# Kernel tuning notes

Hardware: AMD Instinct MI355X
Metric: run time of the kernel (lower is better)

The kernel has to match this reference:

```python
import jax, jax.numpy as jnp
import numpy as np

HEADS = 16
DIM_HEAD = 64


def setup_inputs() -> dict:
    key = jax.random.key(0)
    k1, k2, k3 = jax.random.split(key, 3)
    b, n, dim = 2, 2048, 1024
    x = jax.random.normal(k1, (b, n, dim), dtype=jnp.float32)
    W_qkv = jax.random.normal(k2, (dim, 6 * HEADS * DIM_HEAD), dtype=jnp.float32) * 0.02
    W_out = jax.random.normal(k3, (HEADS * DIM_HEAD, dim), dtype=jnp.float32) * 0.02
    return {"x": x, "W_qkv": W_qkv, "W_out": W_out}


def reference(x, W_qkv, W_out):
    b, n, _ = x.shape
    h, d = HEADS, DIM_HEAD
    scale = d ** -0.5

    # project and split into 6 head-wise tensors: (qkv h d) grouping order
    qkv = (x @ W_qkv).reshape(b, n, 6, h, d).transpose(2, 0, 3, 1, 4)  # [6,b,h,n,d]
    qu, ku, vu, qc, kc, vc = qkv
    qu_s = qu * scale
    qc_s = qc * scale

    idx = jnp.arange(n)
    future = idx[None, :] > idx[:, None]  # torch triu(1): True strictly above diag

    # term1: qc . vu, zeroed on future positions
    term1 = jnp.einsum('bhid,bhjd->bhij', qc_s, vu)
    term1 = jnp.where(future, 0.0, term1)

    # sigmoid lookahead attention, kept ONLY on strictly-future positions
    lookahead = jax.nn.sigmoid(jnp.einsum('bhid,bhjd->bhij', qu_s, ku))
    lookahead = jnp.where(future, lookahead, 0.0)

    # Su[i,k] = sum_j term1[i,j] * lookahead[k,j]
    Su = jnp.einsum('bhij,bhkj->bhik', term1, lookahead)
    Sc = jnp.einsum('bhid,bhjd->bhij', qc_s, kc)

    scores = Sc - jax.nn.silu(Su)
    neg = -jnp.finfo(scores.dtype).max
    scores = jnp.where(future, neg, scores)

    attn = jax.nn.softmax(scores, axis=-1)
    out = jnp.einsum('bhij,bhjd->bhid', attn, vc)  # [b,h,n,d]

    out = out.transpose(0, 2, 1, 3).reshape(b, n, h * d)
    return out @ W_out
```

## Files before the change

### kernel.cpp

```cpp
#include <hip/hip_runtime.h>
#include <hip/hip_bf16.h>
#include <stdint.h>


typedef unsigned short u16;
typedef __attribute__((ext_vector_type(8))) short s8v;
typedef __attribute__((ext_vector_type(4))) float f4v;

__device__ __forceinline__ u16 f2bf(float f) {
  union { float f; unsigned u; } v; v.f = f;
  unsigned r = v.u + 0x7FFFu + ((v.u >> 16) & 1u);
  return (u16)(r >> 16);
}
__device__ __forceinline__ float bf2f(u16 u) {
  union { unsigned u; float f; } v; v.u = ((unsigned)u) << 16; return v.f;
}

typedef __attribute__((address_space(1))) const void* gas_t;
typedef __attribute__((address_space(3))) void* las_t;
__device__ __forceinline__ void gld16(const void* g, void* l) {
  __builtin_amdgcn_global_load_lds((gas_t)g, (las_t)l, 16, 0, 0);
}

__device__ __forceinline__ void zero_acc(f4v acc[4][4]) {
  f4v z = {0.f, 0.f, 0.f, 0.f};
#pragma unroll
  for (int m = 0; m < 4; ++m)
#pragma unroll
    for (int n = 0; n < 4; ++n) acc[m][n] = z;
}


__global__ void convert_x_kernel(const float* __restrict__ in, u16* __restrict__ out) {
  int i = (blockIdx.x * 256 + threadIdx.x) * 4;
  float4 v = *(const float4*)(&in[i]);
  out[i + 0] = f2bf(v.x);
  out[i + 1] = f2bf(v.y);
  out[i + 2] = f2bf(v.z);
  out[i + 3] = f2bf(v.w);
}

__global__ void transpose_convert_kernel(const float* __restrict__ in, u16* __restrict__ out,
                                         int R, int C) {
  __shared__ float tile[32][33];
  int c0 = blockIdx.x * 32, r0 = blockIdx.y * 32;
  for (int rr = threadIdx.y; rr < 32; rr += 8)
    tile[rr][threadIdx.x] = in[(size_t)(r0 + rr) * C + (c0 + threadIdx.x)];
  __syncthreads();
  for (int cc = threadIdx.y; cc < 32; cc += 8)
    out[(size_t)(c0 + cc) * R + (r0 + threadIdx.x)] = f2bf(tile[threadIdx.x][cc]);
}


__global__ __launch_bounds__(256, 2) void gemm_qkv_kernel(
    const u16* __restrict__ xb, const u16* __restrict__ wqkvT,
    u16* __restrict__ quS, u16* __restrict__ ku, u16* __restrict__ vu,
    u16* __restrict__ qcS, u16* __restrict__ kc, u16* __restrict__ vcN) {
  __shared__ u16 sA[2][8192];
  __shared__ u16 sB[2][8192];
  int bm = blockIdx.x, bn = blockIdx.y;
  int tid = threadIdx.x, lane = tid & 63, w = tid >> 6, wm = w >> 1, wn = w & 1;
  int g = lane >> 4, l15 = lane & 15;
  const int sz = (l15 & 7) << 3;
  const int bo = tid * 16;

  const u16* Ab = xb + (size_t)(bm * 128) * 1024;
  const u16* Bb = wqkvT + (size_t)(bn * 128) * 1024;

  auto stg = [&](const u16* base, int ks, u16* dst) {
#pragma unroll
    for (int it = 0; it < 4; ++it) {
      int o = bo + it * 4096;
      int row = o >> 7, lo = o & 127;
      gld16(base + (size_t)row * 1024 + ks * 64 + ((lo ^ ((row & 7) << 4)) >> 1),
            (char*)dst + o);
    }
  };

  f4v acc[4][4];
  zero_acc(acc);
  stg(Ab, 0, sA[0]);
  stg(Bb, 0, sB[0]);
  stg(Ab, 1, sA[1]);
  stg(Bb, 1, sB[1]);

  for (int ks = 0; ks < 16; ++ks) {
    int buf = ks & 1;
    if (ks < 15)
      asm volatile("s_waitcnt vmcnt(8)" ::: "memory");
    else
      asm volatile("s_waitcnt vmcnt(0)" ::: "memory");
    __builtin_amdgcn_sched_barrier(0);
    __builtin_amdgcn_s_barrier();
    __builtin_amdgcn_sched_barrier(0);
#pragma unroll
    for (int kk = 0; kk < 2; ++kk) {
      int c2 = kk * 32 + g * 8;
      s8v a[4], b[4];
#pragma unroll
      for (int m = 0; m < 4; ++m)
        a[m] = *(const s8v*)(&sA[buf][(wm * 64 + m * 16 + l15) * 64 + (c2 ^ sz)]);
#pragma unroll
      for (int n = 0; n < 4; ++n)
        b[n] = *(const s8v*)(&sB[buf][(wn * 64 + n * 16 + l15) * 64 + (c2 ^ sz)]);
#pragma unroll
      for (int m = 0; m < 4; ++m)
#pragma unroll
        for (int n = 0; n < 4; ++n)
          acc[m][n] = __builtin_amdgcn_mfma_f32_16x16x32_bf16(a[m], b[n], acc[m][n], 0, 0, 0);
    }
    __builtin_amdgcn_s_barrier();
    if (ks + 2 < 16) {
      stg(Ab, ks + 2, sA[buf]);
      stg(Bb, ks + 2, sB[buf]);
    }
  }

  int s = bn >> 3;
  int b = bm >> 4;
  int nn0 = (bm & 15) * 128;
  int hh0 = (bn & 7) * 2;
  float scale = (s == 0 || s == 3) ? 0.125f : 1.f;
  u16* obase;
  switch (s) {
    case 0: obase = quS; break;
    case 1: obase = ku; break;
    case 2: obase = vu; break;
    case 3: obase = qcS; break;
    case 4: obase = kc; break;
    default: obase = vcN; break;
  }
  u16* sE = (u16*)sA;
#pragma unroll
  for (int pass = 0; pass < 2; ++pass) {
    __syncthreads();
    if (wn == pass) {
#pragma unroll
      for (int m = 0; m < 4; ++m)
#pragma unroll
        for (int n = 0; n < 4; ++n)
#pragma unroll
          for (int j = 0; j < 4; ++j) {
            int lrow = wm * 64 + m * 16 + g * 4 + j;
            int d = n * 16 + l15;
            sE[lrow * 64 + d] = f2bf(acc[m][n][j] * scale);
          }
    }
    __syncthreads();
    int bh = (b << 4) + hh0 + pass;
    u16* dst = obase + ((size_t)bh * 2048 + nn0) * 64;
    for (int it = 0; it < 4; ++it) {
      int e = (tid + it * 256) * 8;
      *(uint4*)(dst + e) = *(const uint4*)(&sE[e]);
    }
  }
}


__global__ __launch_bounds__(256) void transpose_v_kernel(const u16* __restrict__ vcN,
                                                          u16* __restrict__ vcT) {
  __shared__ u16 t[64][72];
  int nt = blockIdx.x, bh = blockIdx.y;
  const u16* src = vcN + ((size_t)bh * 2048 + nt * 64) * 64;
  int tid = threadIdx.x;
  for (int i = tid; i < 512; i += 256) {
    int r = i >> 3, cseg = i & 7;
    *(uint4*)(&t[r][cseg * 8]) = *(const uint4*)(src + r * 64 + cseg * 8);
  }
  __syncthreads();
  u16* dst = vcT + (size_t)bh * 64 * 2048 + nt * 64;
  for (int i = tid; i < 512; i += 256) {
    int d = i >> 3, nseg = i & 7;
    u16 tmp[8];
#pragma unroll
    for (int e = 0; e < 8; ++e) tmp[e] = t[nseg * 8 + e][d];
    *(uint4*)(dst + (size_t)d * 2048 + nseg * 8) = *(uint4*)tmp;
  }
}


__global__ __launch_bounds__(256, 2) void tl_kernel(
    const u16* __restrict__ qcS, const u16* __restrict__ vu,
    const u16* __restrict__ quS, const u16* __restrict__ ku,
    u16* __restrict__ term1p, u16* __restrict__ lookp, int c0) {
  __shared__ u16 S[32768];
  int t = blockIdx.x, lb = blockIdx.y, bh = c0 + lb;
  int I = 0;
  while ((I + 1) * (I + 2) / 2 <= t) ++I;
  int K = t - I * (I + 1) / 2;
  int tid = threadIdx.x, lane = tid & 63, w = tid >> 6, wm = w >> 1, wn = w & 1;
  int g = lane >> 4, l15 = lane & 15;
  const int sz = (l15 & 7) << 3;
  const int bo = tid * 16;

  auto stg = [&](const u16* base, int rt, u16* dst) {
#pragma unroll
    for (int it = 0; it < 4; ++it) {
      int o = bo + it * 4096;
      int row = o >> 7, lo = o & 127;
      gld16(base + ((size_t)bh * 2048 + rt * 128 + row) * 64 + ((lo ^ ((row & 7) << 4)) >> 1),
            (char*)dst + o);
    }
  };
  stg(qcS, I, S);
  stg(vu, K, S + 8192);
  stg(quS, K, S + 16384);
  stg(ku, I, S + 24576);

  asm volatile("s_waitcnt vmcnt(0)" ::: "memory");
  __builtin_amdgcn_sched_barrier(0);
  __syncthreads();

  f4v acc1[4][4], acc2[4][4];
  zero_acc(acc1);
  zero_acc(acc2);
#pragma unroll
  for (int kk = 0; kk < 2; ++kk) {
    int c2 = kk * 32 + g * 8;
    s8v a1[4], b1[4], a2[4], b2[4];
#pragma unroll
    for (int m = 0; m < 4; ++m) {
      a1[m] = *(const s8v*)(&S[(wm * 64 + m * 16 + l15) * 64 + (c2 ^ sz)]);
      a2[m] = *(const s8v*)(&S[16384 + (wm * 64 + m * 16 + l15) * 64 + (c2 ^ sz)]);
    }
#pragma unroll
    for (int n = 0; n < 4; ++n) {
      b1[n] = *(const s8v*)(&S[8192 + (wn * 64 + n * 16 + l15) * 64 + (c2 ^ sz)]);
      b2[n] = *(const s8v*)(&S[24576 + (wn * 64 + n * 16 + l15) * 64 + (c2 ^ sz)]);
    }
#pragma unroll
    for (int m = 0; m < 4; ++m)
#pragma unroll
      for (int n = 0; n < 4; ++n) {
        acc1[m][n] = __builtin_amdgcn_mfma_f32_16x16x32_bf16(a1[m], b1[n], acc1[m][n], 0, 0, 0);
        acc2[m][n] = __builtin_amdgcn_mfma_f32_16x16x32_bf16(a2[m], b2[n], acc2[m][n], 0, 0, 0);
      }
  }
  __syncthreads();

#pragma unroll
  for (int m = 0; m < 4; ++m)
#pragma unroll
    for (int n = 0; n < 4; ++n)
#pragma unroll
      for (int j4 = 0; j4 < 4; ++j4) {
        int lr = wm * 64 + m * 16 + g * 4 + j4;
        int lc = wn * 64 + n * 16 + l15;
        int idx = wn * 8192 + lr * 64 + ((lc & 63) ^ ((lr & 7) << 3));
        float v1 = acc1[m][n][j4];
        v1 = ((K * 128 + lc) > (I * 128 + lr)) ? 0.f : v1;
        S[idx] = f2bf(v1);
        float v2 = acc2[m][n][j4];
        v2 = ((I * 128 + lc) > (K * 128 + lr)) ? (1.f / (1.f + __expf(-v2))) : 0.f;
        S[16384 + idx] = f2bf(v2);
      }
  __syncthreads();

  u16* o1 = term1p + ((size_t)lb * 136 + t) * 16384;
  u16* o2 = lookp + ((size_t)lb * 136 + t) * 16384;
#pragma unroll
  for (int it = 0; it < 8; ++it) {
    int e = (tid + it * 256) * 8;
    *(uint4*)(o1 + e) = *(const uint4*)(&S[e]);
    *(uint4*)(o2 + e) = *(const uint4*)(&S[16384 + e]);
  }
}


__global__ __launch_bounds__(256, 2) void castle_kernel(
    const u16* __restrict__ term1p, const u16* __restrict__ lookp,
    const u16* __restrict__ qcS, const u16* __restrict__ kc,
    const u16* __restrict__ vcT,
    u16* __restrict__ opart, float* __restrict__ ml, int c0) {
  __shared__ u16 sA[16384];
  __shared__ u16 sB[16384];
  int bid = blockIdx.x;
  int lb = bid / 136, sid = bid % 136;
  int bh = c0 + lb;
  int I = 15, rem = sid;
  while (rem > I) { rem -= I + 1; --I; }
  int K = rem;
  int t = I * (I + 1) / 2 + K;

  int tid = threadIdx.x, lane = tid & 63, w = tid >> 6;
  int g = lane >> 4, l15 = lane & 15;
  const int sz = (l15 & 7) << 3;

  const char* t1b = (const char*)(term1p + (size_t)lb * 136 * 16384);
  const char* lkb = (const char*)(lookp + (size_t)lb * 136 * 16384);
  const int IT = I * (I + 1) / 2;
  const int bo = tid * 16;

  s8v qa[2][2];
#pragma unroll
  for (int mg = 0; mg < 2; ++mg)
#pragma unroll
    for (int kk = 0; kk < 2; ++kk)
      qa[mg][kk] = *(const s8v*)(&qcS[((size_t)bh * 2048 + I * 128 + w * 32 + mg * 16 + l15) * 64 +
                                      kk * 32 + g * 8]);

  f4v su[2][8];
  {
    f4v z = {0.f, 0.f, 0.f, 0.f};
#pragma unroll
    for (int mg = 0; mg < 2; ++mg)
#pragma unroll
      for (int n = 0; n < 8; ++n) su[mg][n] = z;
  }

  auto stage = [&](int h, int buf) {
    int j = h >> 1, hf = h & 1;
    const char* srcA = t1b + (size_t)(IT + j) * 32768 + hf * 16384;
    const char* srcB = lkb + (size_t)(j * (j + 1) / 2 + K) * 32768 + hf * 16384;
    char* dA = (char*)sA + buf * 16384;
    char* dB = (char*)sB + buf * 16384;
#pragma unroll
    for (int it = 0; it < 4; ++it) {
      gld16(srcA + bo + it * 4096, dA + bo + it * 4096);
      gld16(srcB + bo + it * 4096, dB + bo + it * 4096);
    }
  };

  const int h0 = 2 * K, h1 = 2 * I + 1;
  stage(h0, 0);
  for (int h = h0; h <= h1; ++h) {
    int cur = (h - h0) & 1;
    if (h < h1) {
      stage(h + 1, cur ^ 1);
      asm volatile("s_waitcnt vmcnt(8)" ::: "memory");
    } else {
      asm volatile("s_waitcnt vmcnt(0)" ::: "memory");
    }
    __builtin_amdgcn_sched_barrier(0);
    __builtin_amdgcn_s_barrier();
    __builtin_amdgcn_sched_barrier(0);
    const u16* bA = sA + cur * 8192;
    const u16* bB = sB + cur * 8192;
    __builtin_amdgcn_s_setprio(1);
#pragma unroll
    for (int kk = 0; kk < 2; ++kk) {
      int c2 = kk * 32 + g * 8;
      s8v a[2], b[8];
      a[0] = *(const s8v*)(&bA[(w * 32 + l15) * 64 + (c2 ^ sz)]);
      a[1] = *(const s8v*)(&bA[(w * 32 + 16 + l15) * 64 + (c2 ^ sz)]);
#pragma unroll
      for (int n = 0; n < 8; ++n)
        b[n] = *(const s8v*)(&bB[(n * 16 + l15) * 64 + (c2 ^ sz)]);
#pragma unroll
      for (int mg = 0; mg < 2; ++mg)
#pragma unroll
        for (int n = 0; n < 8; ++n)
          su[mg][n] = __builtin_amdgcn_mfma_f32_16x16x32_bf16(a[mg], b[n], su[mg][n], 0, 0, 0);
    }
    __builtin_amdgcn_s_setprio(0);
    __builtin_amdgcn_s_barrier();
  }

  {
#pragma unroll
    for (int it = 0; it < 4; ++it) {
      int o = bo + it * 4096;
      int kh = o >> 13, oc = o & 8191;
      int dr = oc >> 7, lo = oc & 127;
      const u16* src = vcT + ((size_t)bh * 64 + dr) * 2048 + K * 128 + kh * 64 +
                       ((lo ^ ((dr & 7) << 4)) >> 1);
      gld16(src, (char*)sB + o);
    }
#pragma unroll
    for (int it = 0; it < 4; ++it) {
      int o = bo + it * 4096;
      int row = o >> 7, lo = o & 127;
      const u16* src = kc + ((size_t)bh * 2048 + K * 128 + row) * 64 +
                       ((lo ^ ((row & 7) << 4)) >> 1);
      gld16(src, (char*)sB + 16384 + o);
    }
  }
#pragma unroll
  for (int mg = 0; mg < 2; ++mg)
#pragma unroll
    for (int n = 0; n < 8; ++n)
#pragma unroll
      for (int j4 = 0; j4 < 4; ++j4) {
        float xv = su[mg][n][j4];
        su[mg][n][j4] = -(xv / (1.f + __expf(-xv)));
      }
  __syncthreads();

#pragma unroll
  for (int kk = 0; kk < 2; ++kk) {
    int c = kk * 32 + g * 8;
    s8v b[8];
#pragma unroll
    for (int n = 0; n < 8; ++n)
      b[n] = *(const s8v*)(&sB[8192 + (n * 16 + l15) * 64 + (c ^ sz)]);
#pragma unroll
    for (int mg = 0; mg < 2; ++mg)
#pragma unroll
      for (int n = 0; n < 8; ++n)
        su[mg][n] = __builtin_amdgcn_mfma_f32_16x16x32_bf16(qa[mg][kk], b[n], su[mg][n], 0, 0, 0);
  }

  if (K == I) {
#pragma unroll
    for (int mg = 0; mg < 2; ++mg)
#pragma unroll
      for (int n = 0; n < 8; ++n)
#pragma unroll
        for (int j4 = 0; j4 < 4; ++j4) {
          int lr = w * 32 + mg * 16 + g * 4 + j4;
          int lc = n * 16 + l15;
          if (lc > lr) su[mg][n][j4] = -3.0e38f;
        }
  }

  float mrow[2][4], lrow[2][4];
#pragma unroll
  for (int mg = 0; mg < 2; ++mg)
#pragma unroll
    for (int j4 = 0; j4 < 4; ++j4) {
      float v = -3.0e38f;
#pragma unroll
      for (int n = 0; n < 8; ++n) v = fmaxf(v, su[mg][n][j4]);
      v = fmaxf(v, __shfl_xor(v, 1));
      v = fmaxf(v, __shfl_xor(v, 2));
      v = fmaxf(v, __shfl_xor(v, 4));
      v = fmaxf(v, __shfl_xor(v, 8));
      mrow[mg][j4] = v;
    }
#pragma unroll
  for (int mg = 0; mg < 2; ++mg)
#pragma unroll
    for (int j4 = 0; j4 < 4; ++j4) {
      float sum = 0.f;
      int prow = w * 32 + mg * 16 + g * 4 + j4;
      int psz = ((g * 4 + j4) & 7) << 3;
#pragma unroll
      for (int n = 0; n < 8; ++n) {
        float e = __expf(su[mg][n][j4] - mrow[mg][j4]);
        sum += e;
        int pc = n * 16 + l15;
        sA[(n >> 2) * 8192 + prow * 64 + ((pc & 63) ^ psz)] = f2bf(e);
      }
      sum += __shfl_xor(sum, 1);
      sum += __shfl_xor(sum, 2);
      sum += __shfl_xor(sum, 4);
      sum += __shfl_xor(sum, 8);
      lrow[mg][j4] = sum;
    }
  __syncthreads();

  f4v o[2][4];
  {
    f4v z = {0.f, 0.f, 0.f, 0.f};
#pragma unroll
    for (int mg = 0; mg < 2; ++mg)
#pragma unroll
      for (int nd = 0; nd < 4; ++nd) o[mg][nd] = z;
  }
#pragma unroll
  for (int kk = 0; kk < 4; ++kk) {
    int kh = kk >> 1;
    int cc = (kk & 1) * 32 + g * 8;
    s8v pa[2], vb[4];
#pragma unroll
    for (int mg = 0; mg < 2; ++mg)
      pa[mg] = *(const s8v*)(&sA[kh * 8192 + (w * 32 + mg * 16 + l15) * 64 + (cc ^ sz)]);
#pragma unroll
    for (int nd = 0; nd < 4; ++nd)
      vb[nd] = *(const s8v*)(&sB[kh * 4096 + (nd * 16 + l15) * 64 + (cc ^ sz)]);
#pragma unroll
    for (int mg = 0; mg < 2; ++mg)
#pragma unroll
      for (int nd = 0; nd < 4; ++nd)
        o[mg][nd] = __builtin_amdgcn_mfma_f32_16x16x32_bf16(pa[mg], vb[nd], o[mg][nd], 0, 0, 0);
  }

  size_t tb = (size_t)lb * 136 + t;
#pragma unroll
  for (int mg = 0; mg < 2; ++mg)
#pragma unroll
    for (int nd = 0; nd < 4; ++nd)
#pragma unroll
      for (int j4 = 0; j4 < 4; ++j4) {
        int prow = w * 32 + mg * 16 + g * 4 + j4;
        int dcol = nd * 16 + l15;
        opart[(tb * 128 + prow) * 64 + dcol] = f2bf(o[mg][nd][j4]);
      }
  if (l15 == 0) {
#pragma unroll
    for (int mg = 0; mg < 2; ++mg)
#pragma unroll
      for (int j4 = 0; j4 < 4; ++j4) {
        int prow = w * 32 + mg * 16 + g * 4 + j4;
        ml[tb * 256 + prow] = mrow[mg][j4];
        ml[tb * 256 + 128 + prow] = lrow[mg][j4];
      }
  }
}


__global__ __launch_bounds__(256) void combine_kernel(const u16* __restrict__ opart,
                                                      const float* __restrict__ ml,
                                                      u16* __restrict__ attn, int c0) {
  int lb = blockIdx.x, I = blockIdx.y, bh = c0 + lb;
  int tid = threadIdx.x;
  int row = tid >> 1, dh = (tid & 1) << 5;
  float M = -3.0e38f, L = 0.f;
  float O[32];
#pragma unroll
  for (int i = 0; i < 32; ++i) O[i] = 0.f;
  for (int K = 0; K <= I; ++K) {
    size_t tb = (size_t)lb * 136 + I * (I + 1) / 2 + K;
    float m = ml[tb * 256 + row];
    float l = ml[tb * 256 + 128 + row];
    float newM = fmaxf(M, m);
    float so = __expf(M - newM), sn = __expf(m - newM);
    L = L * so + l * sn;
    const u16* op = opart + (tb * 128 + row) * 64 + dh;
#pragma unroll
    for (int q = 0; q < 4; ++q) {
      s8v ov = *(const s8v*)(op + q * 8);
#pragma unroll
      for (int e = 0; e < 8; ++e)
        O[q * 8 + e] = O[q * 8 + e] * so + bf2f((u16)ov[e]) * sn;
    }
    M = newM;
  }
  float inv = 1.f / L;
  int b = bh >> 4, hh = bh & 15;
  u16* dst = attn + ((size_t)b * 2048 + I * 128 + row) * 1024 + hh * 64 + dh;
#pragma unroll
  for (int i = 0; i < 32; ++i) dst[i] = f2bf(O[i] * inv);
}


__global__ __launch_bounds__(256, 2) void gemm_out_kernel(const u16* __restrict__ attn,
                                                          const u16* __restrict__ woutT,
                                                          float* __restrict__ out) {
  __shared__ u16 sA[2][8192];
  __shared__ u16 sB[2][8192];
  int bm = blockIdx.x, bn = blockIdx.y;
  int tid = threadIdx.x, lane = tid & 63, w = tid >> 6, wm = w >> 1, wn = w & 1;
  int g = lane >> 4, l15 = lane & 15;
  const int sz = (l15 & 7) << 3;
  const int bo = tid * 16;

  const u16* Ab = attn + (size_t)(bm * 128) * 1024;
  const u16* Bb = woutT + (size_t)(bn * 128) * 1024;

  auto stg = [&](const u16* base, int ks, u16* dst) {
#pragma unroll
    for (int it = 0; it < 4; ++it) {
      int o = bo + it * 4096;
      int row = o >> 7, lo = o & 127;
      gld16(base + (size_t)row * 1024 + ks * 64 + ((lo ^ ((row & 7) << 4)) >> 1),
            (char*)dst + o);
    }
  };

  f4v acc[4][4];
  zero_acc(acc);
  stg(Ab, 0, sA[0]);
  stg(Bb, 0, sB[0]);
  stg(Ab, 1, sA[1]);
  stg(Bb, 1, sB[1]);

  for (int ks = 0; ks < 16; ++ks) {
    int buf = ks & 1;
    if (ks < 15)
      asm volatile("s_waitcnt vmcnt(8)" ::: "memory");
    else
      asm volatile("s_waitcnt vmcnt(0)" ::: "memory");
    __builtin_amdgcn_sched_barrier(0);
    __builtin_amdgcn_s_barrier();
    __builtin_amdgcn_sched_barrier(0);
#pragma unroll
    for (int kk = 0; kk < 2; ++kk) {
      int c2 = kk * 32 + g * 8;
      s8v a[4], b[4];
#pragma unroll
      for (int m = 0; m < 4; ++m)
        a[m] = *(const s8v*)(&sA[buf][(wm * 64 + m * 16 + l15) * 64 + (c2 ^ sz)]);
#pragma unroll
      for (int n = 0; n < 4; ++n)
        b[n] = *(const s8v*)(&sB[buf][(wn * 64 + n * 16 + l15) * 64 + (c2 ^ sz)]);
#pragma unroll
      for (int m = 0; m < 4; ++m)
#pragma unroll
        for (int n = 0; n < 4; ++n)
          acc[m][n] = __builtin_amdgcn_mfma_f32_16x16x32_bf16(a[m], b[n], acc[m][n], 0, 0, 0);
    }
    __builtin_amdgcn_s_barrier();
    if (ks + 2 < 16) {
      stg(Ab, ks + 2, sA[buf]);
      stg(Bb, ks + 2, sB[buf]);
    }
  }

#pragma unroll
  for (int m = 0; m < 4; ++m)
#pragma unroll
    for (int n = 0; n < 4; ++n)
#pragma unroll
      for (int j = 0; j < 4; ++j) {
        int row = bm * 128 + wm * 64 + m * 16 + g * 4 + j;
        int col = bn * 128 + wn * 64 + n * 16 + l15;
        out[(size_t)row * 1024 + col] = acc[m][n][j];
      }
}


extern "C" void kernel_launch(void* const* d_in, const int* in_sizes, int n_in,
                              void* d_out, int out_size, void* d_ws, size_t ws_size,
                              hipStream_t stream) {
  const float* x = (const float*)d_in[0];
  const float* Wqkv = (const float*)d_in[1];
  const float* Wout = (const float*)d_in[2];
  float* out = (float*)d_out;

  char* base = (char*)d_ws;
  size_t off = 0;
  auto alloc = [&](size_t bytes) -> void* {
    void* p = base + off;
    off += (bytes + 255) & ~(size_t)255;
    return p;
  };

  u16* woutT = (u16*)alloc(1024ull * 1024 * 2);
  u16* quS = (u16*)alloc(32ull * 2048 * 64 * 2);
  u16* ku = (u16*)alloc(32ull * 2048 * 64 * 2);
  u16* vu = (u16*)alloc(32ull * 2048 * 64 * 2);
  u16* qcS = (u16*)alloc(32ull * 2048 * 64 * 2);
  u16* kc = (u16*)alloc(32ull * 2048 * 64 * 2);
  u16* vcN = (u16*)alloc(32ull * 2048 * 64 * 2);
  u16* vcT = (u16*)alloc(32ull * 2048 * 64 * 2);
  u16* attn = (u16*)alloc(4096ull * 1024 * 2);

  size_t perBH = 136ull * 16384 * 2 * 2 + 136ull * 128 * 64 * 2 + 136ull * 256 * 4;
  size_t remain = (ws_size > off) ? (ws_size - off) : 0;
  int chunk = (int)(remain / perBH);
  if (chunk < 1) chunk = 1;
  if (chunk > 32) chunk = 32;
  u16* term1p = (u16*)alloc((size_t)chunk * 136 * 16384 * 2);
  u16* lookp = (u16*)alloc((size_t)chunk * 136 * 16384 * 2);
  u16* opart = (u16*)alloc((size_t)chunk * 136 * 8192 * 2);
  float* mlb = (float*)alloc((size_t)chunk * 136 * 256 * 4);

  u16* xb;
  u16* wqkvT;
  if ((size_t)chunk * 136 * 16384 * 2 >= (4096ull + 6144ull) * 1024 * 2) {
    xb = term1p;
    wqkvT = term1p + 4096ull * 1024;
  } else {
    xb = (u16*)alloc(4096ull * 1024 * 2);
    wqkvT = (u16*)alloc(6144ull * 1024 * 2);
  }

  convert_x_kernel<<<4096, 256, 0, stream>>>(x, xb);
  transpose_convert_kernel<<<dim3(192, 32), dim3(32, 8), 0, stream>>>(Wqkv, wqkvT, 1024, 6144);
  transpose_convert_kernel<<<dim3(32, 32), dim3(32, 8), 0, stream>>>(Wout, woutT, 1024, 1024);
  gemm_qkv_kernel<<<dim3(32, 48), 256, 0, stream>>>(xb, wqkvT, quS, ku, vu, qcS, kc, vcN);
  transpose_v_kernel<<<dim3(32, 32), 256, 0, stream>>>(vcN, vcT);

  for (int c0 = 0; c0 < 32; c0 += chunk) {
    int nb = (32 - c0 < chunk) ? (32 - c0) : chunk;
    tl_kernel<<<dim3(136, nb), 256, 0, stream>>>(qcS, vu, quS, ku, term1p, lookp, c0);
    castle_kernel<<<dim3(136 * nb), 256, 0, stream>>>(term1p, lookp, qcS, kc, vcT, opart, mlb, c0);
    combine_kernel<<<dim3(nb, 16), 256, 0, stream>>>(opart, mlb, attn, c0);
  }
  gemm_out_kernel<<<dim3(32, 8), 256, 0, stream>>>(attn, woutT, out);
}
```

Measured before the change: 500.3 us.

## Enlarge castle tiles to 256x256 with 512-thread blocks and zero-tile padding

Each castle block now covers a 256x256 output region built from 2x2 of the old 128x128 tiles, using 8 waves and a 128KB shared buffer. Each staged term1 and lookahead tile is therefore reused across twice as many output rows and columns, which cuts global and LDS traffic per MFMA. Missing triangle tiles are replaced by loads from a zeroed scratch tile. The P matrix is written into per-wave LDS slices, dropping one block-wide barrier. The cost is some wasted MFMA work on the diagonal blocks, one block per CU, higher register pressure, and fewer blocks in the grid.

Result: no change. 496.1 us (-0.8%).

```diff
diff --git a/kernel.cpp b/kernel.cpp
--- a/kernel.cpp
+++ b/kernel.cpp
@@ -267,61 +267,68 @@
 }
 
 
-__global__ __launch_bounds__(256, 2) void castle_kernel(
+__global__ __launch_bounds__(512, 1) void castle_kernel(
     const u16* __restrict__ term1p, const u16* __restrict__ lookp,
     const u16* __restrict__ qcS, const u16* __restrict__ kc,
-    const u16* __restrict__ vcT,
+    const u16* __restrict__ vcT, const u16* __restrict__ ztile,
     u16* __restrict__ opart, float* __restrict__ ml, int c0) {
-  __shared__ u16 sA[16384];
-  __shared__ u16 sB[16384];
+  __shared__ u16 S[65536];
   int bid = blockIdx.x;
-  int lb = bid / 136, sid = bid % 136;
+  int lb = bid / 36, sid = bid % 36;
   int bh = c0 + lb;
-  int I = 15, rem = sid;
-  while (rem > I) { rem -= I + 1; --I; }
-  int K = rem;
-  int t = I * (I + 1) / 2 + K;
+  int d = 7, rem = sid;
+  while (rem >= 8 - d) { rem -= 8 - d; --d; }
+  int Kp = rem, Ip = Kp + d;
 
   int tid = threadIdx.x, lane = tid & 63, w = tid >> 6;
   int g = lane >> 4, l15 = lane & 15;
   const int sz = (l15 & 7) << 3;
+  int rhalf = w >> 2, rsub = w & 3;
+  int i_t = 2 * Ip + rhalf;
+  int rowbase = rsub * 32;
+  const int bo = tid * 16;
 
   const char* t1b = (const char*)(term1p + (size_t)lb * 136 * 16384);
   const char* lkb = (const char*)(lookp + (size_t)lb * 136 * 16384);
-  const int IT = I * (I + 1) / 2;
-  const int bo = tid * 16;
 
   s8v qa[2][2];
 #pragma unroll
   for (int mg = 0; mg < 2; ++mg)
 #pragma unroll
     for (int kk = 0; kk < 2; ++kk)
-      qa[mg][kk] = *(const s8v*)(&qcS[((size_t)bh * 2048 + I * 128 + w * 32 + mg * 16 + l15) * 64 +
-                                      kk * 32 + g * 8]);
-
-  f4v su[2][8];
+      qa[mg][kk] = *(const s8v*)(&qcS[((size_t)bh * 2048 + i_t * 128 + rowbase + mg * 16 + l15) *
+                                          64 + kk * 32 + g * 8]);
+
+  f4v su[2][16];
   {
     f4v z = {0.f, 0.f, 0.f, 0.f};
 #pragma unroll
     for (int mg = 0; mg < 2; ++mg)
 #pragma unroll
-      for (int n = 0; n < 8; ++n) su[mg][n] = z;
+      for (int n = 0; n < 16; ++n) su[mg][n] = z;
   }
 
   auto stage = [&](int h, int buf) {
-    int j = h >> 1, hf = h & 1;
-    const char* srcA = t1b + (size_t)(IT + j) * 32768 + hf * 16384;
-    const char* srcB = lkb + (size_t)(j * (j + 1) / 2 + K) * 32768 + hf * 16384;
-    char* dA = (char*)sA + buf * 16384;
-    char* dB = (char*)sB + buf * 16384;
-#pragma unroll
-    for (int it = 0; it < 4; ++it) {
-      gld16(srcA + bo + it * 4096, dA + bo + it * 4096);
-      gld16(srcB + bo + it * 4096, dB + bo + it * 4096);
+    int jt = h >> 1, hf = h & 1;
+    const char* a0 = (jt <= 2 * Ip)
+                         ? t1b + (size_t)(2 * Ip * (2 * Ip + 1) / 2 + jt) * 32768 + hf * 16384
+                         : (const char*)ztile;
+    const char* a1 = t1b + (size_t)((2 * Ip + 1) * (2 * Ip + 2) / 2 + jt) * 32768 + hf * 16384;
+    const char* b0 = lkb + (size_t)(jt * (jt + 1) / 2 + 2 * Kp) * 32768 + hf * 16384;
+    const char* b1 = (jt >= 2 * Kp + 1)
+                         ? lkb + (size_t)(jt * (jt + 1) / 2 + 2 * Kp + 1) * 32768 + hf * 16384
+                         : (const char*)ztile;
+    char* dst = (char*)S + buf * 65536;
+#pragma unroll
+    for (int r = 0; r < 2; ++r) {
+      gld16(a0 + bo + r * 8192, dst + bo + r * 8192);
+      gld16(a1 + bo + r * 8192, dst + 16384 + bo + r * 8192);
+      gld16(b0 + bo + r * 8192, dst + 32768 + bo + r * 8192);
+      gld16(b1 + bo + r * 8192, dst + 49152 + bo + r * 8192);
     }
   };
 
-  const int h0 = 2 * K, h1 = 2 * I + 1;
+  const int h0 = 4 * Kp, h1 = 4 * Ip + 3;
   stage(h0, 0);
   for (int h = h0; h <= h1; ++h) {
     int cur = (h - h0) & 1;
@@ -334,23 +341,21 @@
     __builtin_amdgcn_sched_barrier(0);
     __builtin_amdgcn_s_barrier();
     __builtin_amdgcn_sched_barrier(0);
-    const u16* bA = sA + cur * 8192;
-    const u16* bB = sB + cur * 8192;
+    const u16* TA = S + cur * 32768 + rhalf * 8192;
+    const u16* LB = S + cur * 32768 + 16384;
     __builtin_amdgcn_s_setprio(1);
 #pragma unroll
     for (int kk = 0; kk < 2; ++kk) {
       int c2 = kk * 32 + g * 8;
-      s8v a[2], b[8];
-      a[0] = *(const s8v*)(&bA[(w * 32 + l15) * 64 + (c2 ^ sz)]);
-      a[1] = *(const s8v*)(&bA[(w * 32 + 16 + l15) * 64 + (c2 ^ sz)]);
-#pragma unroll
-      for (int n = 0; n < 8; ++n)
-        b[n] = *(const s8v*)(&bB[(n * 16 + l15) * 64 + (c2 ^ sz)]);
-#pragma unroll
-      for (int mg = 0; mg < 2; ++mg)
-#pragma unroll
-        for (int n = 0; n < 8; ++n)
-          su[mg][n] = __builtin_amdgcn_mfma_f32_16x16x32_bf16(a[mg], b[n], su[mg][n], 0, 0, 0);
+      s8v a[2];
+      a[0] = *(const s8v*)(&TA[(rowbase + l15) * 64 + (c2 ^ sz)]);
+      a[1] = *(const s8v*)(&TA[(rowbase + 16 + l15) * 64 + (c2 ^ sz)]);
+#pragma unroll
+      for (int n = 0; n < 16; ++n) {
+        s8v b = *(const s8v*)(&LB[(n >> 3) * 8192 + ((n & 7) * 16 + l15) * 64 + (c2 ^ sz)]);
+        su[0][n] = __builtin_amdgcn_mfma_f32_16x16x32_bf16(a[0], b, su[0][n], 0, 0, 0);
+        su[1][n] = __builtin_amdgcn_mfma_f32_16x16x32_bf16(a[1], b, su[1][n], 0, 0, 0);
+      }
     }
     __builtin_amdgcn_s_setprio(0);
     __builtin_amdgcn_s_barrier();
@@ -359,26 +364,26 @@
   {
 #pragma unroll
     for (int it = 0; it < 4; ++it) {
-      int o = bo + it * 4096;
-      int kh = o >> 13, oc = o & 8191;
+      int o = bo + it * 8192;
+      int row = o >> 7, lo = o & 127;
+      const u16* src = kc + ((size_t)bh * 2048 + Kp * 256 + row) * 64 +
+                       ((lo ^ ((row & 7) << 4)) >> 1);
+      gld16(src, (char*)S + o);
+    }
+#pragma unroll
+    for (int it = 0; it < 4; ++it) {
+      int o = bo + it * 8192;
+      int kq = o >> 13, oc = o & 8191;
       int dr = oc >> 7, lo = oc & 127;
-      const u16* src = vcT + ((size_t)bh * 64 + dr) * 2048 + K * 128 + kh * 64 +
+      const u16* src = vcT + ((size_t)bh * 64 + dr) * 2048 + Kp * 256 + kq * 64 +
                        ((lo ^ ((dr & 7) << 4)) >> 1);
-      gld16(src, (char*)sB + o);
-    }
-#pragma unroll
-    for (int it = 0; it < 4; ++it) {
-      int o = bo + it * 4096;
-      int row = o >> 7, lo = o & 127;
-      const u16* src = kc + ((size_t)bh * 2048 + K * 128 + row) * 64 +
-                       ((lo ^ ((row & 7) << 4)) >> 1);
-      gld16(src, (char*)sB + 16384 + o);
+      gld16(src, (char*)S + 32768 + o);
     }
   }
 #pragma unroll
   for (int mg = 0; mg < 2; ++mg)
 #pragma unroll
-    for (int n = 0; n < 8; ++n)
+    for (int n = 0; n < 16; ++n)
 #pragma unroll
       for (int j4 = 0; j4 < 4; ++j4) {
         float xv = su[mg][n][j4];
@@ -389,29 +394,24 @@
 #pragma unroll
   for (int kk = 0; kk < 2; ++kk) {
     int c = kk * 32 + g * 8;
-    s8v b[8];
-#pragma unroll
-    for (int n = 0; n < 8; ++n)
-      b[n] = *(const s8v*)(&sB[8192 + (n * 16 + l15) * 64 + (c ^ sz)]);
-#pragma unroll
-    for (int mg = 0; mg < 2; ++mg)
-#pragma unroll
-      for (int n = 0; n < 8; ++n)
-        su[mg][n] = __builtin_amdgcn_mfma_f32_16x16x32_bf16(qa[mg][kk], b[n], su[mg][n], 0, 0, 0);
-  }
-
-  if (K == I) {
-#pragma unroll
-    for (int mg = 0; mg < 2; ++mg)
-#pragma unroll
-      for (int n = 0; n < 8; ++n)
-#pragma unroll
-        for (int j4 = 0; j4 < 4; ++j4) {
-          int lr = w * 32 + mg * 16 + g * 4 + j4;
-          int lc = n * 16 + l15;
-          if (lc > lr) su[mg][n][j4] = -3.0e38f;
-        }
-  }
+#pragma unroll
+    for (int n = 0; n < 16; ++n) {
+      s8v b = *(const s8v*)(&S[(n * 16 + l15) * 64 + (c ^ sz)]);
+      su[0][n] = __builtin_amdgcn_mfma_f32_16x16x32_bf16(qa[0][kk], b, su[0][n], 0, 0, 0);
+      su[1][n] = __builtin_amdgcn_mfma_f32_16x16x32_bf16(qa[1][kk], b, su[1][n], 0, 0, 0);
+    }
+  }
+
+#pragma unroll
+  for (int mg = 0; mg < 2; ++mg)
+#pragma unroll
+    for (int n = 0; n < 16; ++n)
+#pragma unroll
+      for (int j4 = 0; j4 < 4; ++j4) {
+        int grow = i_t * 128 + rowbase + mg * 16 + g * 4 + j4;
+        int gcol = Kp * 256 + n * 16 + l15;
+        if (gcol > grow) su[mg][n][j4] = -3.0e38f;
+      }
 
   float mrow[2][4], lrow[2][4];
 #pragma unroll
@@ -420,26 +420,18 @@
     for (int j4 = 0; j4 < 4; ++j4) {
       float v = -3.0e38f;
 #pragma unroll
-      for (int n = 0; n < 8; ++n) v = fmaxf(v, su[mg][n][j4]);
+      for (int n = 0; n < 16; ++n) v = fmaxf(v, su[mg][n][j4]);
       v = fmaxf(v, __shfl_xor(v, 1));
       v = fmaxf(v, __shfl_xor(v, 2));
       v = fmaxf(v, __shfl_xor(v, 4));
       v = fmaxf(v, __shfl_xor(v, 8));
       mrow[mg][j4] = v;
-    }
-#pragma unroll
-  for (int mg = 0; mg < 2; ++mg)
-#pragma unroll
-    for (int j4 = 0; j4 < 4; ++j4) {
       float sum = 0.f;
-      int prow = w * 32 + mg * 16 + g * 4 + j4;
-      int psz = ((g * 4 + j4) & 7) << 3;
-#pragma unroll
-      for (int n = 0; n < 8; ++n) {
-        float e = __expf(su[mg][n][j4] - mrow[mg][j4]);
+#pragma unroll
+      for (int n = 0; n < 16; ++n) {
+        float e = __expf(su[mg][n][j4] - v);
+        su[mg][n][j4] = e;
         sum += e;
-        int pc = n * 16 + l15;
-        sA[(n >> 2) * 8192 + prow * 64 + ((pc & 63) ^ psz)] = f2bf(e);
       }
       sum += __shfl_xor(sum, 1);
       sum += __shfl_xor(sum, 2);
@@ -447,7 +439,6 @@
       sum += __shfl_xor(sum, 8);
       lrow[mg][j4] = sum;
     }
-  __syncthreads();
 
   f4v o[2][4];
   {
@@ -457,32 +448,48 @@
 #pragma unroll
       for (int nd = 0; nd < 4; ++nd) o[mg][nd] = z;
   }
-#pragma unroll
-  for (int kk = 0; kk < 4; ++kk) {
-    int kh = kk >> 1;
-    int cc = (kk & 1) * 32 + g * 8;
-    s8v pa[2], vb[4];
+  u16* Pw = S + 32768 + w * 2048;
+#pragma unroll
+  for (int kq = 0; kq < 4; ++kq) {
 #pragma unroll
     for (int mg = 0; mg < 2; ++mg)
-      pa[mg] = *(const s8v*)(&sA[kh * 8192 + (w * 32 + mg * 16 + l15) * 64 + (cc ^ sz)]);
+#pragma unroll
+      for (int j4 = 0; j4 < 4; ++j4) {
+        int rl = mg * 16 + g * 4 + j4;
+        int psz = (rl & 7) << 3;
+#pragma unroll
+        for (int nn = 0; nn < 4; ++nn) {
+          int pc = nn * 16 + l15;
+          Pw[rl * 64 + (pc ^ psz)] = f2bf(su[mg][kq * 4 + nn][j4]);
+        }
+      }
+    asm volatile("s_waitcnt lgkmcnt(0)" ::: "memory");
+    __builtin_amdgcn_sched_barrier(0);
+#pragma unroll
+    for (int kk = 0; kk < 2; ++kk) {
+      int c = kk * 32 + g * 8;
+      s8v pa[2], vb[4];
+      pa[0] = *(const s8v*)(&Pw[(l15) * 64 + (c ^ sz)]);
+      pa[1] = *(const s8v*)(&Pw[(16 + l15) * 64 + (c ^ sz)]);
+#pragma unroll
+      for (int nd = 0; nd < 4; ++nd)
+        vb[nd] = *(const s8v*)(&S[16384 + kq * 4096 + (nd * 16 + l15) * 64 + (c ^ sz)]);
+#pragma unroll
+      for (int mg = 0; mg < 2; ++mg)
+#pragma unroll
+        for (int nd = 0; nd < 4; ++nd)
+          o[mg][nd] = __builtin_amdgcn_mfma_f32_16x16x32_bf16(pa[mg], vb[nd], o[mg][nd], 0, 0, 0);
+    }
+  }
+
+  size_t tb = (size_t)lb * 128 + i_t * 8 + Kp;
+#pragma unroll
+  for (int mg = 0; mg < 2; ++mg)
 #pragma unroll
     for (int nd = 0; nd < 4; ++nd)
-      vb[nd] = *(const s8v*)(&sB[kh * 4096 + (nd * 16 + l15) * 64 + (cc ^ sz)]);
-#pragma unroll
-    for (int mg = 0; mg < 2; ++mg)
-#pragma unroll
-      for (int nd = 0; nd < 4; ++nd)
-        o[mg][nd] = __builtin_amdgcn_mfma_f32_16x16x32_bf16(pa[mg], vb[nd], o[mg][nd], 0, 0, 0);
-  }
-
-  size_t tb = (size_t)lb * 136 + t;
-#pragma unroll
-  for (int mg = 0; mg < 2; ++mg)
-#pragma unroll
-    for (int nd = 0; nd < 4; ++nd)
 #pragma unroll
       for (int j4 = 0; j4 < 4; ++j4) {
-        int prow = w * 32 + mg * 16 + g * 4 + j4;
+        int prow = rowbase + mg * 16 + g * 4 + j4;
         int dcol = nd * 16 + l15;
         opart[(tb * 128 + prow) * 64 + dcol] = f2bf(o[mg][nd][j4]);
       }
@@ -491,7 +498,7 @@
     for (int mg = 0; mg < 2; ++mg)
 #pragma unroll
       for (int j4 = 0; j4 < 4; ++j4) {
-        int prow = w * 32 + mg * 16 + g * 4 + j4;
+        int prow = rowbase + mg * 16 + g * 4 + j4;
         ml[tb * 256 + prow] = mrow[mg][j4];
         ml[tb * 256 + 128 + prow] = lrow[mg][j4];
       }
@@ -509,8 +516,9 @@
   float O[32];
 #pragma unroll
   for (int i = 0; i < 32; ++i) O[i] = 0.f;
-  for (int K = 0; K <= I; ++K) {
-    size_t tb = (size_t)lb * 136 + I * (I + 1) / 2 + K;
+  int kmax = I >> 1;
+  for (int K = 0; K <= kmax; ++K) {
+    size_t tb = (size_t)lb * 128 + I * 8 + K;
     float m = ml[tb * 256 + row];
     float l = ml[tb * 256 + 128 + row];
     float newM = fmaxf(M, m);
@@ -635,16 +643,17 @@
   u16* vcN = (u16*)alloc(32ull * 2048 * 64 * 2);
   u16* vcT = (u16*)alloc(32ull * 2048 * 64 * 2);
   u16* attn = (u16*)alloc(4096ull * 1024 * 2);
-
-  size_t perBH = 136ull * 16384 * 2 * 2 + 136ull * 128 * 64 * 2 + 136ull * 256 * 4;
+  u16* ztile = (u16*)alloc(16384);
+
+  size_t perBH = 136ull * 16384 * 2 * 2 + 128ull * 128 * 64 * 2 + 128ull * 256 * 4;
   size_t remain = (ws_size > off) ? (ws_size - off) : 0;
   int chunk = (int)(remain / perBH);
   if (chunk < 1) chunk = 1;
   if (chunk > 32) chunk = 32;
   u16* term1p = (u16*)alloc((size_t)chunk * 136 * 16384 * 2);
   u16* lookp = (u16*)alloc((size_t)chunk * 136 * 16384 * 2);
-  u16* opart = (u16*)alloc((size_t)chunk * 136 * 8192 * 2);
-  float* mlb = (float*)alloc((size_t)chunk * 136 * 256 * 4);
+  u16* opart = (u16*)alloc((size_t)chunk * 128 * 8192 * 2);
+  float* mlb = (float*)alloc((size_t)chunk * 128 * 256 * 4);
 
   u16* xb;
   u16* wqkvT;
@@ -656,6 +665,7 @@
     wqkvT = (u16*)alloc(6144ull * 1024 * 2);
   }
 
+  hipMemsetAsync(ztile, 0, 16384, stream);
   convert_x_kernel<<<4096, 256, 0, stream>>>(x, xb);
   transpose_convert_kernel<<<dim3(192, 32), dim3(32, 8), 0, stream>>>(Wqkv, wqkvT, 1024, 6144);
   transpose_convert_kernel<<<dim3(32, 32), dim3(32, 8), 0, stream>>>(Wout, woutT, 1024, 1024);
@@ -665,7 +675,8 @@
   for (int c0 = 0; c0 < 32; c0 += chunk) {
     int nb = (32 - c0 < chunk) ? (32 - c0) : chunk;
     tl_kernel<<<dim3(136, nb), 256, 0, stream>>>(qcS, vu, quS, ku, term1p, lookp, c0);
-    castle_kernel<<<dim3(136 * nb), 256, 0, stream>>>(term1p, lookp, qcS, kc, vcT, opart, mlb, c0);
+    castle_kernel<<<dim3(36 * nb), 512, 0, stream>>>(term1p, lookp, qcS, kc, vcT, ztile,
+                                                     opart, mlb, c0);
     combine_kernel<<<dim3(nb, 16), 256, 0, stream>>>(opart, mlb, attn, c0);
   }
   gemm_out_kernel<<<dim3(32, 8), 256, 0, stream>>>(attn, woutT, out);
```
